# Kernel optimization log

Hardware: AMD Instinct MI355X
Metric: run time of the kernel (lower is better)

The kernel has to match this reference:

```python
import math
import jax, jax.numpy as jnp
import numpy as np

B, N, D = 4, 4096, 1024
H, DH = 16, 64  # D == H * DH


def setup_inputs() -> dict:
    key = jax.random.key(0)
    ks = jax.random.split(key, 7)
    s = 1.0 / math.sqrt(D)
    return {
        "tens": jax.random.normal(ks[0], (B, N, D), dtype=jnp.float32),
        "Wq": jax.random.normal(ks[1], (D, D), dtype=jnp.float32) * s,
        "bq": jax.random.normal(ks[2], (D,), dtype=jnp.float32) * 0.01,
        "Wk": jax.random.normal(ks[3], (D, D), dtype=jnp.float32) * s,
        "bk": jax.random.normal(ks[4], (D,), dtype=jnp.float32) * 0.01,
        "Wv": jax.random.normal(ks[5], (D, D), dtype=jnp.float32) * s,
        "bv": jax.random.normal(ks[6], (D,), dtype=jnp.float32) * 0.01,
    }


def reference(tens, Wq, bq, Wk, bk, Wv, bv):
    b, n, d = tens.shape
    # projections (torch Linear: x @ W^T + b)
    q = (tens @ Wq.T + bq).reshape(b, n, H, DH)  # [B,N,H,DH]
    k = (tens @ Wk.T + bk).reshape(b, n, H, DH)
    v = (tens @ Wv.T + bv).reshape(b, n, H, DH)
    scale = (1.0 / math.sqrt(DH)) / math.sqrt(n)
    # No softmax between QK^T and V => linear, reassociate as Q @ (K^T V)
    # to avoid the O(N^2) attention matrix; identical math.
    ktv = jnp.einsum("bnhd,bnhe->bhde", k, v)          # [B,H,DH,DH]
    out = jnp.einsum("bnhd,bhde->bnhe", q, ktv) * scale  # [B,N,H,DH]
    return out.reshape(b, n, d)
```

## Files before the change

### kernel.cpp

```cpp
#include <hip/hip_runtime.h>

typedef unsigned short ushort_t;
typedef __attribute__((ext_vector_type(8))) __bf16 bf16x8;
typedef __attribute__((ext_vector_type(8))) unsigned short ushort8;
typedef __attribute__((ext_vector_type(4))) float floatx4;

__device__ inline unsigned short f2bf(float f) {
  union { float f; unsigned u; } x; x.f = f;
  return (unsigned short)((x.u + 0x7FFFu + ((x.u >> 16) & 1u)) >> 16);
}

__global__ void cvt_f32_bf16(const float* __restrict__ in, ushort_t* __restrict__ out, int n) {
  int i = (blockIdx.x * blockDim.x + threadIdx.x) * 8;
  if (i >= n) return;
  const float4* p = (const float4*)(in + i);
  float4 a = p[0], b = p[1];
  ushort8 o;
  o[0] = f2bf(a.x); o[1] = f2bf(a.y); o[2] = f2bf(a.z); o[3] = f2bf(a.w);
  o[4] = f2bf(b.x); o[5] = f2bf(b.y); o[6] = f2bf(b.z); o[7] = f2bf(b.w);
  *(ushort8*)(out + i) = o;
}

__device__ inline void gload_lds16(const void* g, void* l) {
  __builtin_amdgcn_global_load_lds(
      (const __attribute__((address_space(1))) unsigned int*)g,
      (__attribute__((address_space(3))) unsigned int*)l, 16, 0, 0);
}

__device__ inline void store_out(float* p, float v) { *p = v; }
__device__ inline void store_out(ushort_t* p, float v) { *p = f2bf(v); }

template <typename OutT>
__global__ void gemm_bt(const ushort_t* __restrict__ A, const ushort_t* __restrict__ Bm,
                        const float* __restrict__ bias, OutT* __restrict__ C,
                        int M, int N, long sA_, long sB_, long sBias_, long sC_) {
  const int K = 1024;

  int gx = gridDim.x, gxy = gridDim.x * gridDim.y;
  int flat = blockIdx.x + gx * blockIdx.y + gxy * blockIdx.z;
  int total = gxy * gridDim.z;
  int per = total >> 3;
  int nf = (flat & 7) * per + (flat >> 3);
  int bz = nf / gxy; int rem = nf - bz * gxy;
  int by = rem / gx; int bx = rem - by * gx;

  A += (long)bz * sA_; Bm += (long)bz * sB_; bias += (long)bz * sBias_; C += (long)bz * sC_;

  __shared__ ushort_t sA[128 * 32];
  __shared__ ushort_t sB[128 * 32];

  int t = threadIdx.x;
  int w = t >> 6, l = t & 63;
  int wy = w >> 1, wx = w & 1;
  int quad = l >> 4, m16 = l & 15;
  int mBase = by * 128, nBase = bx * 128;

  int r = l >> 2, pb = l & 3;
  int swzS = (r ^ (r >> 2)) & 3;
  int sRow0 = w * 32 + r;
  int sCol = (pb ^ swzS) * 8;
  const ushort_t* gA0 = A + (long)(mBase + sRow0) * K + sCol;
  const ushort_t* gA1 = gA0 + 16 * K;
  const ushort_t* gB0 = Bm + (long)(nBase + sRow0) * K + sCol;
  const ushort_t* gB1 = gB0 + 16 * K;
  ushort_t* lA0 = sA + (w * 2) * 512;
  ushort_t* lA1 = lA0 + 512;
  ushort_t* lB0 = sB + (w * 2) * 512;
  ushort_t* lB1 = lB0 + 512;

  int swzR = (m16 ^ (m16 >> 2)) & 3;
  int aOff = (wy * 64 + m16) * 32 + (quad ^ swzR) * 8;
  int bOff = (wx * 64 + m16) * 32 + (quad ^ swzR) * 8;

  floatx4 acc[4][4] = {};

  for (int kt = 0; kt < K; kt += 32) {
    __syncthreads();
    gload_lds16(gA0 + kt, lA0);
    gload_lds16(gA1 + kt, lA1);
    gload_lds16(gB0 + kt, lB0);
    gload_lds16(gB1 + kt, lB1);
    __syncthreads();
    bf16x8 af[4], bfr[4];
#pragma unroll
    for (int i = 0; i < 4; ++i) af[i] = *(const bf16x8*)(sA + aOff + i * 16 * 32);
#pragma unroll
    for (int i = 0; i < 4; ++i) bfr[i] = *(const bf16x8*)(sB + bOff + i * 16 * 32);
#pragma unroll
    for (int mi = 0; mi < 4; ++mi)
#pragma unroll
      for (int ni = 0; ni < 4; ++ni)
        acc[mi][ni] = __builtin_amdgcn_mfma_f32_16x16x32_bf16(af[mi], bfr[ni], acc[mi][ni], 0, 0, 0);
  }

#pragma unroll
  for (int ni = 0; ni < 4; ++ni) {
    int n = nBase + wx * 64 + ni * 16 + m16;
    float bb = bias[n];
#pragma unroll
    for (int mi = 0; mi < 4; ++mi) {
      int m0 = mBase + wy * 64 + mi * 16 + quad * 4;
      floatx4 v = acc[mi][ni];
#pragma unroll
      for (int rr = 0; rr < 4; ++rr)
        store_out(&C[(long)(m0 + rr) * N + n], v[rr] + bb);
    }
  }
}

__global__ void ktv_mfma(const ushort_t* __restrict__ Kb, const ushort_t* __restrict__ Vb,
                         float* __restrict__ part) {
  int bh = blockIdx.x, sl = blockIdx.y;
  int b = bh >> 4, h = bh & 15;
  __shared__ ushort_t sKT[64 * 40];
  __shared__ ushort_t sVT[64 * 40];
  int t = threadIdx.x;
  int w = t >> 6, l = t & 63;
  int quad = l >> 4, m16 = l & 15;
  int nr = t & 31, d0 = (t >> 5) * 8;
  long base = ((long)(b * 4096 + sl * 512)) * 1024 + h * 64;
  floatx4 acc[4] = {};
  for (int nc = 0; nc < 512; nc += 32) {
    __syncthreads();
    ushort8 kv = *(const ushort8*)(Kb + base + (long)(nc + nr) * 1024 + d0);
    ushort8 vv = *(const ushort8*)(Vb + base + (long)(nc + nr) * 1024 + d0);
#pragma unroll
    for (int i = 0; i < 8; ++i) {
      sKT[(d0 + i) * 40 + nr] = kv[i];
      sVT[(d0 + i) * 40 + nr] = vv[i];
    }
    __syncthreads();
    bf16x8 af = *(const bf16x8*)(sKT + (w * 16 + m16) * 40 + quad * 8);
#pragma unroll
    for (int j = 0; j < 4; ++j) {
      bf16x8 bf = *(const bf16x8*)(sVT + (j * 16 + m16) * 40 + quad * 8);
      acc[j] = __builtin_amdgcn_mfma_f32_16x16x32_bf16(af, bf, acc[j], 0, 0, 0);
    }
  }
  float* p = part + ((long)(bh * 8 + sl)) * 4096;
#pragma unroll
  for (int j = 0; j < 4; ++j)
#pragma unroll
    for (int rr = 0; rr < 4; ++rr)
      p[(w * 16 + quad * 4 + rr) * 64 + j * 16 + m16] = acc[j][rr];
}

__global__ void ktv_reduce(const float* __restrict__ part, float* __restrict__ ktv) {
  int i = blockIdx.x * 256 + threadIdx.x;
  int bh = i >> 12, de = i & 4095;
  float s = 0.f;
#pragma unroll
  for (int sl = 0; sl < 8; ++sl) s += part[((long)(bh * 8 + sl)) * 4096 + de];
  ktv[i] = s;
}

__global__ void make_w2(const float* __restrict__ Wq, const float* __restrict__ bq,
                        const float* __restrict__ ktv, ushort_t* __restrict__ W2T,
                        float* __restrict__ bias2, float scale) {
  int bh = blockIdx.x, cq = blockIdx.y;
  int b = bh >> 4, h = bh & 15;
  __shared__ float sKTV[64 * 64];
  __shared__ float sW[64 * 64];
  int t = threadIdx.x;
  for (int i = t * 4; i < 4096; i += 1024)
    *(float4*)(sKTV + i) = *(const float4*)(ktv + (long)bh * 4096 + i);
  __syncthreads();
  if (cq == 0 && t < 64) {
    float s = 0.f;
    for (int d = 0; d < 64; ++d) s += bq[h * 64 + d] * sKTV[d * 64 + t];
    bias2[b * 1024 + h * 64 + t] = s * scale;
  }
  int e = t >> 2, c0 = (t & 3) * 16;
  for (int ct = cq * 256; ct < cq * 256 + 256; ct += 64) {
    __syncthreads();
    {
      int d = t >> 2, cc = (t & 3) * 16;
#pragma unroll
      for (int j = 0; j < 16; j += 4)
        *(float4*)(sW + d * 64 + cc + j) =
            *(const float4*)(Wq + (long)(h * 64 + d) * 1024 + ct + cc + j);
    }
    __syncthreads();
    float outv[16] = {};
    for (int d = 0; d < 64; ++d) {
      float kv = sKTV[d * 64 + e];
#pragma unroll
      for (int j = 0; j < 16; ++j) outv[j] += sW[d * 64 + c0 + j] * kv;
    }
    ushort8 o0, o1;
#pragma unroll
    for (int j = 0; j < 8; ++j) { o0[j] = f2bf(outv[j] * scale); o1[j] = f2bf(outv[8 + j] * scale); }
    ushort_t* dst = W2T + ((long)(b * 1024 + h * 64 + e)) * 1024 + ct + c0;
    *(ushort8*)dst = o0;
    *(ushort8*)(dst + 8) = o1;
  }
}

extern "C" void kernel_launch(void* const* d_in, const int* in_sizes, int n_in,
                              void* d_out, int out_size, void* d_ws, size_t ws_size,
                              hipStream_t stream) {
  (void)in_sizes; (void)n_in; (void)out_size; (void)ws_size;
  const float* tens = (const float*)d_in[0];
  const float* Wq = (const float*)d_in[1];
  const float* bq = (const float*)d_in[2];
  const float* Wk = (const float*)d_in[3];
  const float* bk = (const float*)d_in[4];
  const float* Wv = (const float*)d_in[5];
  const float* bv = (const float*)d_in[6];
  float* out = (float*)d_out;

  char* w = (char*)d_ws;
  ushort_t* Xbf  = (ushort_t*)(w);
  ushort_t* Kbf  = (ushort_t*)(w + 33554432);
  ushort_t* Vbf  = (ushort_t*)(w + 67108864);
  ushort_t* Wkbf = (ushort_t*)(w + 100663296);
  ushort_t* Wvbf = (ushort_t*)(w + 102760448);
  float*    part = (float*)(w + 104857600);
  float*    ktv  = (float*)(w + 113246208);
  ushort_t* W2T  = (ushort_t*)(w + 114294784);
  float*    bias2= (float*)(w + 122683392);

  const float scale = (1.0f / 8.0f) / 64.0f;

  hipLaunchKernelGGL(cvt_f32_bf16, dim3(8192), dim3(256), 0, stream, tens, Xbf, 16777216);
  hipLaunchKernelGGL(cvt_f32_bf16, dim3(512), dim3(256), 0, stream, Wk, Wkbf, 1048576);
  hipLaunchKernelGGL(cvt_f32_bf16, dim3(512), dim3(256), 0, stream, Wv, Wvbf, 1048576);

  hipLaunchKernelGGL((gemm_bt<ushort_t>), dim3(8, 128, 1), dim3(256), 0, stream,
                     Xbf, Wkbf, bk, Kbf, 16384, 1024, 0L, 0L, 0L, 0L);
  hipLaunchKernelGGL((gemm_bt<ushort_t>), dim3(8, 128, 1), dim3(256), 0, stream,
                     Xbf, Wvbf, bv, Vbf, 16384, 1024, 0L, 0L, 0L, 0L);

  hipLaunchKernelGGL(ktv_mfma, dim3(64, 8), dim3(256), 0, stream, Kbf, Vbf, part);
  hipLaunchKernelGGL(ktv_reduce, dim3(1024), dim3(256), 0, stream, part, ktv);
  hipLaunchKernelGGL(make_w2, dim3(64, 4), dim3(256), 0, stream, Wq, bq, ktv, W2T, bias2, scale);

  hipLaunchKernelGGL((gemm_bt<float>), dim3(8, 32, 4), dim3(256), 0, stream,
                     Xbf, W2T, bias2, out, 4096, 1024,
                     4194304L, 1048576L, 1024L, 4194304L);
}
```

Measured before the change: 309.4 us.

## Compute K^T V via input Gram matrix instead of full K/V projections

Replaces the two full-size K and V projection GEMMs and the K^T V reduction with an algebraic rewrite. It computes the per-batch Gram matrix X^T X from a transposed copy of X, multiplies it by Wk, then by Wv per head. Bias terms are restored with column sums of X and small GEMVs. This removes roughly a third of the projection FLOPs and the large K/V intermediate writes and reads. In exchange it adds a transpose pass, a long-K GEMM with only 256 blocks, and extra bf16 rounding of the Gram and intermediate products.

```diff
diff --git a/kernel.cpp b/kernel.cpp
--- a/kernel.cpp
+++ b/kernel.cpp
@@ -3,11 +3,16 @@
 typedef unsigned short ushort_t;
 typedef __attribute__((ext_vector_type(8))) __bf16 bf16x8;
 typedef __attribute__((ext_vector_type(8))) unsigned short ushort8;
+typedef __attribute__((ext_vector_type(4))) unsigned short ushort4v;
 typedef __attribute__((ext_vector_type(4))) float floatx4;
 
 __device__ inline unsigned short f2bf(float f) {
   union { float f; unsigned u; } x; x.f = f;
   return (unsigned short)((x.u + 0x7FFFu + ((x.u >> 16) & 1u)) >> 16);
+}
+__device__ inline float bf2f(unsigned short u) {
+  union { unsigned u; float f; } x; x.u = ((unsigned)u) << 16;
+  return x.f;
 }
 
 __global__ void cvt_f32_bf16(const float* __restrict__ in, ushort_t* __restrict__ out, int n) {
@@ -30,12 +35,10 @@
 __device__ inline void store_out(float* p, float v) { *p = v; }
 __device__ inline void store_out(ushort_t* p, float v) { *p = f2bf(v); }
 
-template <typename OutT>
+template <typename OutT, bool BIAS, int KK>
 __global__ void gemm_bt(const ushort_t* __restrict__ A, const ushort_t* __restrict__ Bm,
                         const float* __restrict__ bias, OutT* __restrict__ C,
                         int M, int N, long sA_, long sB_, long sBias_, long sC_) {
-  const int K = 1024;
-
   int gx = gridDim.x, gxy = gridDim.x * gridDim.y;
   int flat = blockIdx.x + gx * blockIdx.y + gxy * blockIdx.z;
   int total = gxy * gridDim.z;
@@ -44,7 +47,8 @@
   int bz = nf / gxy; int rem = nf - bz * gxy;
   int by = rem / gx; int bx = rem - by * gx;
 
-  A += (long)bz * sA_; Bm += (long)bz * sB_; bias += (long)bz * sBias_; C += (long)bz * sC_;
+  A += (long)bz * sA_; Bm += (long)bz * sB_; C += (long)bz * sC_;
+  if (BIAS) bias += (long)bz * sBias_;
 
   __shared__ ushort_t sA[128 * 32];
   __shared__ ushort_t sB[128 * 32];
@@ -59,10 +63,10 @@
   int swzS = (r ^ (r >> 2)) & 3;
   int sRow0 = w * 32 + r;
   int sCol = (pb ^ swzS) * 8;
-  const ushort_t* gA0 = A + (long)(mBase + sRow0) * K + sCol;
-  const ushort_t* gA1 = gA0 + 16 * K;
-  const ushort_t* gB0 = Bm + (long)(nBase + sRow0) * K + sCol;
-  const ushort_t* gB1 = gB0 + 16 * K;
+  const ushort_t* gA0 = A + (long)(mBase + sRow0) * KK + sCol;
+  const ushort_t* gA1 = gA0 + 16 * KK;
+  const ushort_t* gB0 = Bm + (long)(nBase + sRow0) * KK + sCol;
+  const ushort_t* gB1 = gB0 + 16 * KK;
   ushort_t* lA0 = sA + (w * 2) * 512;
   ushort_t* lA1 = lA0 + 512;
   ushort_t* lB0 = sB + (w * 2) * 512;
@@ -74,7 +78,7 @@
 
   floatx4 acc[4][4] = {};
 
-  for (int kt = 0; kt < K; kt += 32) {
+  for (int kt = 0; kt < KK; kt += 32) {
     __syncthreads();
     gload_lds16(gA0 + kt, lA0);
     gload_lds16(gA1 + kt, lA1);
@@ -96,7 +100,7 @@
 #pragma unroll
   for (int ni = 0; ni < 4; ++ni) {
     int n = nBase + wx * 64 + ni * 16 + m16;
-    float bb = bias[n];
+    float bb = BIAS ? bias[n] : 0.f;
 #pragma unroll
     for (int mi = 0; mi < 4; ++mi) {
       int m0 = mBase + wy * 64 + mi * 16 + quad * 4;
@@ -108,50 +112,129 @@
   }
 }
 
-__global__ void ktv_mfma(const ushort_t* __restrict__ Kb, const ushort_t* __restrict__ Vb,
-                         float* __restrict__ part) {
-  int bh = blockIdx.x, sl = blockIdx.y;
+__global__ void transpose_bf(const ushort_t* __restrict__ in, ushort_t* __restrict__ out) {
+  int nt = blockIdx.x, ct = blockIdx.y, b = blockIdx.z;
+  __shared__ ushort_t tile[64 * 68];
+  int t = threadIdx.x;
+  int r = t >> 3, c8 = (t & 7) * 8;
+  long ibase = ((long)b * 4096 + nt * 64) * 1024 + (long)ct * 64;
+  ushort8 v0 = *(const ushort8*)(in + ibase + (long)r * 1024 + c8);
+  ushort8 v1 = *(const ushort8*)(in + ibase + (long)(r + 32) * 1024 + c8);
+  ushort4v a0 = {v0[0], v0[1], v0[2], v0[3]}, a1 = {v0[4], v0[5], v0[6], v0[7]};
+  ushort4v b0 = {v1[0], v1[1], v1[2], v1[3]}, b1 = {v1[4], v1[5], v1[6], v1[7]};
+  *(ushort4v*)(tile + r * 68 + c8) = a0;
+  *(ushort4v*)(tile + r * 68 + c8 + 4) = a1;
+  *(ushort4v*)(tile + (r + 32) * 68 + c8) = b0;
+  *(ushort4v*)(tile + (r + 32) * 68 + c8 + 4) = b1;
+  __syncthreads();
+  int c = t >> 3, n0 = (t & 7) * 8;
+#pragma unroll
+  for (int half = 0; half < 2; ++half) {
+    int cc = c + half * 32;
+    ushort8 o;
+#pragma unroll
+    for (int i = 0; i < 8; ++i) o[i] = tile[(n0 + i) * 68 + cc];
+    *(ushort8*)(out + ((long)b * 1024 + ct * 64 + cc) * 4096 + nt * 64 + n0) = o;
+  }
+}
+
+__global__ void colsum(const ushort_t* __restrict__ X, float* __restrict__ s) {
+  int b = blockIdx.x, ct = blockIdx.y;
+  int t = threadIdx.x;
+  int c8 = (t & 7) * 8, g = t >> 3;
+  long base = (long)b * 4194304 + (long)ct * 64;
+  float acc[8] = {};
+  for (int n = g * 128; n < g * 128 + 128; ++n) {
+    ushort8 v = *(const ushort8*)(X + base + (long)n * 1024 + c8);
+#pragma unroll
+    for (int i = 0; i < 8; ++i) acc[i] += bf2f(v[i]);
+  }
+  __shared__ float red[32 * 64];
+#pragma unroll
+  for (int i = 0; i < 8; ++i) red[g * 64 + c8 + i] = acc[i];
+  __syncthreads();
+  if (t < 64) {
+    float sum = 0.f;
+#pragma unroll
+    for (int gg = 0; gg < 32; ++gg) sum += red[gg * 64 + t];
+    s[b * 1024 + ct * 64 + t] = sum;
+  }
+}
+
+__global__ void gemv_uw(const ushort_t* __restrict__ Wkbf, const ushort_t* __restrict__ Wvbf,
+                        const float* __restrict__ s, float* __restrict__ u, float* __restrict__ w) {
+  int b = blockIdx.x, rt = blockIdx.y;
+  __shared__ float ss[1024];
+  int t = threadIdx.x;
+  *(float4*)(ss + t * 4) = *(const float4*)(s + b * 1024 + t * 4);
+  __syncthreads();
+  int wv = t >> 6, l = t & 63;
+  int rl = l >> 3, j8 = (l & 7) * 8;
+#pragma unroll
+  for (int m = 0; m < 2; ++m) {
+    const ushort_t* W = m ? Wvbf : Wkbf;
+    float* o = m ? w : u;
+    for (int rb = 0; rb < 128; rb += 32) {
+      int row = rt * 128 + rb + wv * 8 + rl;
+      float acc = 0.f;
+      for (int k = 0; k < 1024; k += 64) {
+        ushort8 wv8 = *(const ushort8*)(W + (long)row * 1024 + k + j8);
+#pragma unroll
+        for (int i = 0; i < 8; ++i) acc += bf2f(wv8[i]) * ss[k + j8 + i];
+      }
+      acc += __shfl_xor(acc, 1);
+      acc += __shfl_xor(acc, 2);
+      acc += __shfl_xor(acc, 4);
+      if ((l & 7) == 0) o[b * 1024 + row] = acc;
+    }
+  }
+}
+
+__global__ void ktv_small(const ushort_t* __restrict__ T1, const ushort_t* __restrict__ Wvbf,
+                          const float* __restrict__ u, const float* __restrict__ w,
+                          const float* __restrict__ bk, const float* __restrict__ bv,
+                          float* __restrict__ ktv) {
+  int bh = blockIdx.x;
   int b = bh >> 4, h = bh & 15;
-  __shared__ ushort_t sKT[64 * 40];
-  __shared__ ushort_t sVT[64 * 40];
-  int t = threadIdx.x;
-  int w = t >> 6, l = t & 63;
+  __shared__ ushort_t sA[64 * 32];
+  __shared__ ushort_t sB[64 * 32];
+  int t = threadIdx.x, wv = t >> 6, l = t & 63;
   int quad = l >> 4, m16 = l & 15;
-  int nr = t & 31, d0 = (t >> 5) * 8;
-  long base = ((long)(b * 4096 + sl * 512)) * 1024 + h * 64;
+  int r = l >> 2, pb = l & 3;
+  int swzS = (r ^ (r >> 2)) & 3;
+  int sCol = (pb ^ swzS) * 8;
+  const ushort_t* gA = T1 + (long)b * 1048576 + (long)(h * 64 + wv * 16 + r) * 1024 + sCol;
+  const ushort_t* gB = Wvbf + (long)(h * 64 + wv * 16 + r) * 1024 + sCol;
+  ushort_t* lA = sA + wv * 512;
+  ushort_t* lB = sB + wv * 512;
+  int swzR = (m16 ^ (m16 >> 2)) & 3;
+  int aOff = (wv * 16 + m16) * 32 + (quad ^ swzR) * 8;
   floatx4 acc[4] = {};
-  for (int nc = 0; nc < 512; nc += 32) {
-    __syncthreads();
-    ushort8 kv = *(const ushort8*)(Kb + base + (long)(nc + nr) * 1024 + d0);
-    ushort8 vv = *(const ushort8*)(Vb + base + (long)(nc + nr) * 1024 + d0);
-#pragma unroll
-    for (int i = 0; i < 8; ++i) {
-      sKT[(d0 + i) * 40 + nr] = kv[i];
-      sVT[(d0 + i) * 40 + nr] = vv[i];
-    }
-    __syncthreads();
-    bf16x8 af = *(const bf16x8*)(sKT + (w * 16 + m16) * 40 + quad * 8);
+  for (int kt = 0; kt < 1024; kt += 32) {
+    __syncthreads();
+    gload_lds16(gA + kt, lA);
+    gload_lds16(gB + kt, lB);
+    __syncthreads();
+    bf16x8 af = *(const bf16x8*)(sA + aOff);
 #pragma unroll
     for (int j = 0; j < 4; ++j) {
-      bf16x8 bf = *(const bf16x8*)(sVT + (j * 16 + m16) * 40 + quad * 8);
+      bf16x8 bf = *(const bf16x8*)(sB + (j * 16 + m16) * 32 + (quad ^ swzR) * 8);
       acc[j] = __builtin_amdgcn_mfma_f32_16x16x32_bf16(af, bf, acc[j], 0, 0, 0);
     }
   }
-  float* p = part + ((long)(bh * 8 + sl)) * 4096;
-#pragma unroll
-  for (int j = 0; j < 4; ++j)
-#pragma unroll
-    for (int rr = 0; rr < 4; ++rr)
-      p[(w * 16 + quad * 4 + rr) * 64 + j * 16 + m16] = acc[j][rr];
-}
-
-__global__ void ktv_reduce(const float* __restrict__ part, float* __restrict__ ktv) {
-  int i = blockIdx.x * 256 + threadIdx.x;
-  int bh = i >> 12, de = i & 4095;
-  float s = 0.f;
-#pragma unroll
-  for (int sl = 0; sl < 8; ++sl) s += part[((long)(bh * 8 + sl)) * 4096 + de];
-  ktv[i] = s;
+  float* p = ktv + (long)bh * 4096;
+#pragma unroll
+  for (int j = 0; j < 4; ++j) {
+    int e = j * 16 + m16;
+    float bve = bv[h * 64 + e];
+    float wpe = w[b * 1024 + h * 64 + e] + 4096.f * bve;
+#pragma unroll
+    for (int rr = 0; rr < 4; ++rr) {
+      int d = wv * 16 + quad * 4 + rr;
+      float corr = u[b * 1024 + h * 64 + d] * bve + bk[h * 64 + d] * wpe;
+      p[d * 64 + e] = acc[j][rr] + corr;
+    }
+  }
 }
 
 __global__ void make_w2(const float* __restrict__ Wq, const float* __restrict__ bq,
@@ -209,16 +292,19 @@
   const float* bv = (const float*)d_in[6];
   float* out = (float*)d_out;
 
-  char* w = (char*)d_ws;
-  ushort_t* Xbf  = (ushort_t*)(w);
-  ushort_t* Kbf  = (ushort_t*)(w + 33554432);
-  ushort_t* Vbf  = (ushort_t*)(w + 67108864);
-  ushort_t* Wkbf = (ushort_t*)(w + 100663296);
-  ushort_t* Wvbf = (ushort_t*)(w + 102760448);
-  float*    part = (float*)(w + 104857600);
-  float*    ktv  = (float*)(w + 113246208);
-  ushort_t* W2T  = (ushort_t*)(w + 114294784);
-  float*    bias2= (float*)(w + 122683392);
+  char* wsp = (char*)d_ws;
+  ushort_t* Xbf  = (ushort_t*)(wsp);
+  ushort_t* XTbf = (ushort_t*)(wsp + 33554432);
+  ushort_t* Gbf  = (ushort_t*)(wsp + 67108864);
+  ushort_t* T1   = (ushort_t*)(wsp + 75497472);
+  ushort_t* Wkbf = (ushort_t*)(wsp + 83886080);
+  ushort_t* Wvbf = (ushort_t*)(wsp + 85983232);
+  ushort_t* W2T  = (ushort_t*)(wsp + 88080384);
+  float*    ktv  = (float*)(wsp + 96468992);
+  float*    s    = (float*)(wsp + 97517568);
+  float*    u    = (float*)(wsp + 97533952);
+  float*    w    = (float*)(wsp + 97550336);
+  float*    bias2= (float*)(wsp + 97566720);
 
   const float scale = (1.0f / 8.0f) / 64.0f;
 
@@ -226,16 +312,23 @@
   hipLaunchKernelGGL(cvt_f32_bf16, dim3(512), dim3(256), 0, stream, Wk, Wkbf, 1048576);
   hipLaunchKernelGGL(cvt_f32_bf16, dim3(512), dim3(256), 0, stream, Wv, Wvbf, 1048576);
 
-  hipLaunchKernelGGL((gemm_bt<ushort_t>), dim3(8, 128, 1), dim3(256), 0, stream,
-                     Xbf, Wkbf, bk, Kbf, 16384, 1024, 0L, 0L, 0L, 0L);
-  hipLaunchKernelGGL((gemm_bt<ushort_t>), dim3(8, 128, 1), dim3(256), 0, stream,
-                     Xbf, Wvbf, bv, Vbf, 16384, 1024, 0L, 0L, 0L, 0L);
-
-  hipLaunchKernelGGL(ktv_mfma, dim3(64, 8), dim3(256), 0, stream, Kbf, Vbf, part);
-  hipLaunchKernelGGL(ktv_reduce, dim3(1024), dim3(256), 0, stream, part, ktv);
+  hipLaunchKernelGGL(transpose_bf, dim3(64, 16, 4), dim3(256), 0, stream, Xbf, XTbf);
+  hipLaunchKernelGGL(colsum, dim3(4, 16), dim3(256), 0, stream, Xbf, s);
+
+  hipLaunchKernelGGL((gemm_bt<ushort_t, false, 4096>), dim3(8, 8, 4), dim3(256), 0, stream,
+                     XTbf, XTbf, (const float*)nullptr, Gbf, 1024, 1024,
+                     4194304L, 4194304L, 0L, 1048576L);
+
+  hipLaunchKernelGGL(gemv_uw, dim3(4, 8), dim3(256), 0, stream, Wkbf, Wvbf, s, u, w);
+
+  hipLaunchKernelGGL((gemm_bt<ushort_t, false, 1024>), dim3(8, 8, 4), dim3(256), 0, stream,
+                     Wkbf, Gbf, (const float*)nullptr, T1, 1024, 1024,
+                     0L, 1048576L, 0L, 1048576L);
+
+  hipLaunchKernelGGL(ktv_small, dim3(64), dim3(256), 0, stream, T1, Wvbf, u, w, bk, bv, ktv);
   hipLaunchKernelGGL(make_w2, dim3(64, 4), dim3(256), 0, stream, Wq, bq, ktv, W2T, bias2, scale);
 
-  hipLaunchKernelGGL((gemm_bt<float>), dim3(8, 32, 4), dim3(256), 0, stream,
+  hipLaunchKernelGGL((gemm_bt<float, true, 1024>), dim3(8, 32, 4), dim3(256), 0, stream,
                      Xbf, W2T, bias2, out, 4096, 1024,
                      4194304L, 1048576L, 1024L, 4194304L);
 }
```

After: 369.0 us. 19.3% more time.
